# Performance work log

Measured on AMD Instinct MI355X. Metric: run time of the kernel, lower is better.

The kernel has to match this reference:

```python
import jax, jax.numpy as jnp
import numpy as np

E = 1024  # dim_model
H = 16    # num_heads
HD = E // H
B, S = 32, 2048
LN_EPS = 1e-5


def setup_inputs() -> dict:
    key = jax.random.key(0)
    ks = jax.random.split(key, 8)
    x = jax.random.normal(ks[0], (B, S, E), dtype=jnp.float32)
    key_padding_mask = jax.random.randint(ks[1], (B, S), 0, 2).astype(jnp.int32)
    # learned seed (xavier_uniform over [1,1,E])
    bound = float(np.sqrt(6.0 / (1 + E)))
    seed = jax.random.uniform(ks[2], (1, 1, E), minval=-bound, maxval=bound, dtype=jnp.float32)
    # MHA params: packed in_proj [3E, E] (q,k,v stacked) + bias, out_proj [E,E]+bias
    w_scale = 1.0 / np.sqrt(E)
    in_proj_w = jax.random.uniform(ks[3], (3 * E, E), minval=-w_scale, maxval=w_scale, dtype=jnp.float32)
    in_proj_b = jnp.zeros((3 * E,), dtype=jnp.float32)
    out_w = jax.random.uniform(ks[4], (E, E), minval=-w_scale, maxval=w_scale, dtype=jnp.float32)
    out_b = jnp.zeros((E,), dtype=jnp.float32)
    ln_g = jnp.ones((E,), dtype=jnp.float32)
    ln_b = jnp.zeros((E,), dtype=jnp.float32)
    return {"x": x, "key_padding_mask": key_padding_mask, "seed": seed,
            "in_proj_w": in_proj_w, "in_proj_b": in_proj_b,
            "out_w": out_w, "out_b": out_b, "ln_g": ln_g, "ln_b": ln_b}


def reference(x, key_padding_mask, seed, in_proj_w, in_proj_b, out_w, out_b, ln_g, ln_b):
    wq, wk, wv = in_proj_w[:E], in_proj_w[E:2 * E], in_proj_w[2 * E:]
    bq, bk, bv = in_proj_b[:E], in_proj_b[E:2 * E], in_proj_b[2 * E:]
    # q from single learned seed: [1,1,E] -> [1,H,1,HD] (broadcast over batch)
    q = (seed @ wq.T + bq).reshape(1, 1, H, HD).transpose(0, 2, 1, 3)
    k = (x @ wk.T + bk).reshape(x.shape[0], -1, H, HD).transpose(0, 2, 1, 3)  # [B,H,S,HD]
    v = (x @ wv.T + bv).reshape(x.shape[0], -1, H, HD).transpose(0, 2, 1, 3)
    scale = 1.0 / jnp.sqrt(jnp.asarray(HD, dtype=x.dtype))
    scores = jnp.einsum('bhqd,bhkd->bhqk', q * scale, k)  # broadcasts q batch dim -> [B,H,1,S]
    pad = (key_padding_mask == 0)[:, None, None, :]  # True = pad
    scores = jnp.where(pad, -jnp.inf, scores)
    attn = jax.nn.softmax(scores, axis=-1)
    ctx = jnp.einsum('bhqk,bhkd->bhqd', attn, v)  # [B,H,1,HD]
    ctx = ctx.transpose(0, 2, 1, 3).reshape(x.shape[0], E)  # squeeze single query
    out = ctx @ out_w.T + out_b
    mu = jnp.mean(out, axis=-1, keepdims=True)
    var = jnp.mean(jnp.square(out - mu), axis=-1, keepdims=True)
    return (out - mu) / jnp.sqrt(var + LN_EPS) * ln_g + ln_b
```

## Files before the change

### kernel.cpp

```cpp
#include <hip/hip_runtime.h>
#include <hip/hip_bf16.h>
#include <math.h>

#define E 1024
#define H 16
#define HD 64
#define B 32
#define S 2048
#define CH 16
#define CTOK (S / CH)
#define BHE (B * H * E)

typedef __attribute__((ext_vector_type(8))) short short8;
typedef __attribute__((ext_vector_type(4))) float f32x4;

__device__ __forceinline__ short f2bf(float f) {
    union { __hip_bfloat16 h; short s; } u;
    u.h = __float2bfloat16(f);
    return u.s;
}

__global__ __launch_bounds__(256) void qproj_kernel(const float* __restrict__ W,
                                                    const float* __restrict__ bqkv,
                                                    const float* __restrict__ seed,
                                                    float* __restrict__ q) {
    int gw = (blockIdx.x * 256 + threadIdx.x) >> 6;
    int lane = threadIdx.x & 63;
    if (gw >= E) return;
    const float4* row = (const float4*)(W + (size_t)gw * E);
    const float4* sd = (const float4*)seed;
    float acc = 0.f;
#pragma unroll
    for (int k = 0; k < 4; ++k) {
        float4 w4 = row[k * 64 + lane];
        float4 s4 = sd[k * 64 + lane];
        acc = fmaf(w4.x, s4.x, acc); acc = fmaf(w4.y, s4.y, acc);
        acc = fmaf(w4.z, s4.z, acc); acc = fmaf(w4.w, s4.w, acc);
    }
#pragma unroll
    for (int off = 32; off > 0; off >>= 1) acc += __shfl_down(acc, off, 64);
    if (lane == 0) q[gw] = acc + bqkv[gw];
}

__global__ __launch_bounds__(256) void uproj_kernel(const float* __restrict__ W,
                                                    const float* __restrict__ q,
                                                    float* __restrict__ u) {
    int h = blockIdx.y;
    int e = blockIdx.x * 256 + threadIdx.x;
    __shared__ float qs[HD];
    if (threadIdx.x < HD) qs[threadIdx.x] = q[h * HD + threadIdx.x];
    __syncthreads();
    const float* Wk = W + ((size_t)(E + h * HD)) * E + e;
    float acc = 0.f;
#pragma unroll 8
    for (int d = 0; d < HD; ++d) acc = fmaf(qs[d], Wk[(size_t)d * E], acc);
    u[h * E + e] = acc * 0.125f;
}

__global__ __launch_bounds__(512, 4) void fused_kernel(const float* __restrict__ x,
                                                       const int* __restrict__ mask,
                                                       const float* __restrict__ u,
                                                       float* __restrict__ part,
                                                       float* __restrict__ mstat,
                                                       float* __restrict__ lstat) {
    int ss = blockIdx.x, b = blockIdx.y;
    __shared__ short uB[H * E];
    __shared__ float sc[CTOK * 16];
    __shared__ int mk[CTOK];
    __shared__ float4 redm[32];
    __shared__ float mxs[16], lls[16];

    int tid = threadIdx.x;
    for (int un = tid; un < 2048; un += 512) {
        int h = un & 15, e8 = un >> 4;
        const float* up = u + (size_t)h * E + e8 * 8;
        short8 v;
#pragma unroll
        for (int j = 0; j < 8; ++j) v[j] = f2bf(up[j]);
        ((short8*)uB)[un] = v;
    }
    if (tid < CTOK) mk[tid] = mask[(size_t)b * S + ss * CTOK + tid];
    __syncthreads();

    int lane = tid & 63, wid = tid >> 6;

    {
        int tl0 = wid * 16;
        int tr = lane & 15;
        int kg = lane >> 4;
        int myTok = tl0 + tr;
        bool live = mk[myTok] != 0;
        const float* xrow = x + ((size_t)b * S + ss * CTOK + myTok) * E + kg * 8;
        const short8* uB8 = (const short8*)uB;

        f32x4 acc = {0.f, 0.f, 0.f, 0.f};
#pragma unroll 4
        for (int st = 0; st < 32; ++st) {
            float4 lo = make_float4(0.f, 0.f, 0.f, 0.f);
            float4 hi = make_float4(0.f, 0.f, 0.f, 0.f);
            if (live) {
                lo = *(const float4*)(xrow + st * 32);
                hi = *(const float4*)(xrow + st * 32 + 4);
            }
            short8 a;
            a[0] = f2bf(lo.x); a[1] = f2bf(lo.y); a[2] = f2bf(lo.z); a[3] = f2bf(lo.w);
            a[4] = f2bf(hi.x); a[5] = f2bf(hi.y); a[6] = f2bf(hi.z); a[7] = f2bf(hi.w);
            short8 bf = uB8[(st * 4 + kg) * 16 + tr];
            acc = __builtin_amdgcn_mfma_f32_16x16x32_bf16(a, bf, acc, 0, 0, 0);
        }
        int r0 = kg * 4;
#pragma unroll
        for (int r = 0; r < 4; ++r)
            sc[(tl0 + r0 + r) * 16 + tr] = acc[r];
    }
    __syncthreads();

    {
        int tok = tid >> 2, hq = tid & 3;
        float4 s4 = *(const float4*)&sc[tok * 16 + hq * 4];
        bool live = mk[tok] != 0;
        float4 sm = live ? s4 : make_float4(-1e30f, -1e30f, -1e30f, -1e30f);
#pragma unroll
        for (int off = 4; off <= 32; off <<= 1) {
            sm.x = fmaxf(sm.x, __shfl_xor(sm.x, off, 64));
            sm.y = fmaxf(sm.y, __shfl_xor(sm.y, off, 64));
            sm.z = fmaxf(sm.z, __shfl_xor(sm.z, off, 64));
            sm.w = fmaxf(sm.w, __shfl_xor(sm.w, off, 64));
        }
        if (lane < 4) redm[wid * 4 + lane] = sm;
        __syncthreads();
        if (tid < 4) {
            float4 mm = redm[tid];
#pragma unroll
            for (int w = 1; w < 8; ++w) {
                float4 v = redm[w * 4 + tid];
                mm.x = fmaxf(mm.x, v.x); mm.y = fmaxf(mm.y, v.y);
                mm.z = fmaxf(mm.z, v.z); mm.w = fmaxf(mm.w, v.w);
            }
            *(float4*)&mxs[tid * 4] = mm;
        }
        __syncthreads();
        float4 mx4 = *(const float4*)&mxs[hq * 4];
        float4 p4 = make_float4(0.f, 0.f, 0.f, 0.f);
        if (live) {
            p4.x = __expf(s4.x - mx4.x);
            p4.y = __expf(s4.y - mx4.y);
            p4.z = __expf(s4.z - mx4.z);
            p4.w = __expf(s4.w - mx4.w);
        }
        *(float4*)&sc[tok * 16 + hq * 4] = p4;
        float4 l4 = p4;
#pragma unroll
        for (int off = 4; off <= 32; off <<= 1) {
            l4.x += __shfl_xor(l4.x, off, 64);
            l4.y += __shfl_xor(l4.y, off, 64);
            l4.z += __shfl_xor(l4.z, off, 64);
            l4.w += __shfl_xor(l4.w, off, 64);
        }
        __syncthreads();
        if (lane < 4) redm[wid * 4 + lane] = l4;
        __syncthreads();
        if (tid < 4) {
            float4 sl = redm[tid];
#pragma unroll
            for (int w = 1; w < 8; ++w) {
                float4 v = redm[w * 4 + tid];
                sl.x += v.x; sl.y += v.y; sl.z += v.z; sl.w += v.w;
            }
            *(float4*)&lls[tid * 4] = sl;
        }
        __syncthreads();
        if (tid < 16) {
            mstat[((size_t)ss * B + b) * H + tid] = mxs[tid];
            lstat[((size_t)ss * B + b) * H + tid] = lls[tid];
        }
    }

    {
        float2 a2[16];
#pragma unroll
        for (int h = 0; h < 16; ++h) a2[h] = make_float2(0.f, 0.f);
        const float* xp = x + ((size_t)b * S + ss * CTOK) * E + wid * 128 + lane * 2;
        const float4* sc4 = (const float4*)sc;
        for (int tok = 0; tok < CTOK; ++tok) {
            if (!mk[tok]) continue;
            float2 xv = *(const float2*)(xp + (size_t)tok * E);
            float4 p0 = sc4[tok * 4 + 0];
            float4 p1 = sc4[tok * 4 + 1];
            float4 p2 = sc4[tok * 4 + 2];
            float4 p3 = sc4[tok * 4 + 3];
            a2[0].x = fmaf(p0.x, xv.x, a2[0].x);   a2[0].y = fmaf(p0.x, xv.y, a2[0].y);
            a2[1].x = fmaf(p0.y, xv.x, a2[1].x);   a2[1].y = fmaf(p0.y, xv.y, a2[1].y);
            a2[2].x = fmaf(p0.z, xv.x, a2[2].x);   a2[2].y = fmaf(p0.z, xv.y, a2[2].y);
            a2[3].x = fmaf(p0.w, xv.x, a2[3].x);   a2[3].y = fmaf(p0.w, xv.y, a2[3].y);
            a2[4].x = fmaf(p1.x, xv.x, a2[4].x);   a2[4].y = fmaf(p1.x, xv.y, a2[4].y);
            a2[5].x = fmaf(p1.y, xv.x, a2[5].x);   a2[5].y = fmaf(p1.y, xv.y, a2[5].y);
            a2[6].x = fmaf(p1.z, xv.x, a2[6].x);   a2[6].y = fmaf(p1.z, xv.y, a2[6].y);
            a2[7].x = fmaf(p1.w, xv.x, a2[7].x);   a2[7].y = fmaf(p1.w, xv.y, a2[7].y);
            a2[8].x = fmaf(p2.x, xv.x, a2[8].x);   a2[8].y = fmaf(p2.x, xv.y, a2[8].y);
            a2[9].x = fmaf(p2.y, xv.x, a2[9].x);   a2[9].y = fmaf(p2.y, xv.y, a2[9].y);
            a2[10].x = fmaf(p2.z, xv.x, a2[10].x); a2[10].y = fmaf(p2.z, xv.y, a2[10].y);
            a2[11].x = fmaf(p2.w, xv.x, a2[11].x); a2[11].y = fmaf(p2.w, xv.y, a2[11].y);
            a2[12].x = fmaf(p3.x, xv.x, a2[12].x); a2[12].y = fmaf(p3.x, xv.y, a2[12].y);
            a2[13].x = fmaf(p3.y, xv.x, a2[13].x); a2[13].y = fmaf(p3.y, xv.y, a2[13].y);
            a2[14].x = fmaf(p3.z, xv.x, a2[14].x); a2[14].y = fmaf(p3.z, xv.y, a2[14].y);
            a2[15].x = fmaf(p3.w, xv.x, a2[15].x); a2[15].y = fmaf(p3.w, xv.y, a2[15].y);
        }
        float* pb = part + ((size_t)ss * B + b) * (H * E) + wid * 128 + lane * 2;
#pragma unroll
        for (int h = 0; h < 16; ++h) *(float2*)(pb + (size_t)h * E) = a2[h];
    }
}

__global__ __launch_bounds__(256) void ctxc_kernel(const float* __restrict__ W,
                                                   const float* __restrict__ bqkv,
                                                   const float* __restrict__ part,
                                                   const float* __restrict__ mstat,
                                                   const float* __restrict__ lstat,
                                                   float* __restrict__ ctx) {
    int cb = blockIdx.x, b = blockIdx.y, t = threadIdx.x;
    int h0 = cb * 4;
    __shared__ float xls[4 * E];
    __shared__ float fs[4][CH];
    __shared__ float linv[4];
    if (t < 4) {
        int h = h0 + t;
        float mv[CH];
        float mg = -1e30f;
#pragma unroll
        for (int c = 0; c < CH; ++c) {
            mv[c] = mstat[((size_t)c * B + b) * H + h];
            mg = fmaxf(mg, mv[c]);
        }
        float l = 0.f;
#pragma unroll
        for (int c = 0; c < CH; ++c) {
            float fc = __expf(mv[c] - mg);
            fs[t][c] = fc;
            l = fmaf(fc, lstat[((size_t)c * B + b) * H + h], l);
        }
        linv[t] = 1.f / l;
    }
    __syncthreads();
    for (int i = t; i < 4 * E / 4; i += 256) {
        int hl = i >> 8, e4 = i & 255;
        float4 s = make_float4(0.f, 0.f, 0.f, 0.f);
#pragma unroll 4
        for (int c = 0; c < CH; ++c) {
            float fc = fs[hl][c];
            float4 v = ((const float4*)part)[(((size_t)c * B + b) * H + h0 + hl) * (E / 4) + e4];
            s.x = fmaf(fc, v.x, s.x); s.y = fmaf(fc, v.y, s.y);
            s.z = fmaf(fc, v.z, s.z); s.w = fmaf(fc, v.w, s.w);
        }
        float li = linv[hl];
        s.x *= li; s.y *= li; s.z *= li; s.w *= li;
        ((float4*)xls)[i] = s;
    }
    __syncthreads();
    int c = cb * 256 + t;
    int h = c >> 6;
    const float4* wr = (const float4*)(W + ((size_t)(2 * E + c)) * E);
    const float4* xl = (const float4*)(xls + (h - h0) * E);
    float acc = bqkv[2 * E + c];
#pragma unroll 4
    for (int e4 = 0; e4 < E / 4; ++e4) {
        float4 w = wr[e4], xv = xl[e4];
        acc = fmaf(w.x, xv.x, acc); acc = fmaf(w.y, xv.y, acc);
        acc = fmaf(w.z, xv.z, acc); acc = fmaf(w.w, xv.w, acc);
    }
    ctx[(size_t)b * E + c] = acc;
}

__global__ __launch_bounds__(256) void outproj_kernel(const float* __restrict__ Wo,
                                                      const float* __restrict__ ob,
                                                      const float* __restrict__ ctx,
                                                      float* __restrict__ outpre) {
    int obk = blockIdx.x, b = blockIdx.y, t = threadIdx.x;
    int o = obk * 256 + t;
    __shared__ float cl[E];
    const float4* cp = (const float4*)(ctx + (size_t)b * E);
    for (int i = t; i < E / 4; i += 256) ((float4*)cl)[i] = cp[i];
    __syncthreads();
    const float4* wr = (const float4*)(Wo + (size_t)o * E);
    const float4* cl4 = (const float4*)cl;
    float acc = ob[o];
#pragma unroll 4
    for (int e4 = 0; e4 < E / 4; ++e4) {
        float4 w = wr[e4], cv = cl4[e4];
        acc = fmaf(w.x, cv.x, acc); acc = fmaf(w.y, cv.y, acc);
        acc = fmaf(w.z, cv.z, acc); acc = fmaf(w.w, cv.w, acc);
    }
    outpre[(size_t)b * E + o] = acc;
}

__global__ __launch_bounds__(256) void ln_kernel(const float* __restrict__ outpre,
                                                 const float* __restrict__ g,
                                                 const float* __restrict__ bb,
                                                 float* __restrict__ out) {
    int b = blockIdx.x, t = threadIdx.x, lane = t & 63, wid = t >> 6;
    const float4* row = (const float4*)(outpre + (size_t)b * E);
    float4 v = row[t];
    float s = v.x + v.y + v.z + v.w;
    float sq = v.x * v.x + v.y * v.y + v.z * v.z + v.w * v.w;
    __shared__ float rs[4], rq[4];
#pragma unroll
    for (int off = 32; off > 0; off >>= 1) {
        s += __shfl_down(s, off, 64);
        sq += __shfl_down(sq, off, 64);
    }
    if (lane == 0) { rs[wid] = s; rq[wid] = sq; }
    __syncthreads();
    s = rs[0] + rs[1] + rs[2] + rs[3];
    sq = rq[0] + rq[1] + rq[2] + rq[3];
    float mean = s * (1.f / E);
    float var = sq * (1.f / E) - mean * mean;
    float inv = rsqrtf(var + 1e-5f);
    float4 gv = ((const float4*)g)[t];
    float4 bv = ((const float4*)bb)[t];
    float4 o;
    o.x = (v.x - mean) * inv * gv.x + bv.x;
    o.y = (v.y - mean) * inv * gv.y + bv.y;
    o.z = (v.z - mean) * inv * gv.z + bv.z;
    o.w = (v.w - mean) * inv * gv.w + bv.w;
    ((float4*)(out + (size_t)b * E))[t] = o;
}

extern "C" void kernel_launch(void* const* d_in, const int* in_sizes, int n_in,
                              void* d_out, int out_size, void* d_ws, size_t ws_size,
                              hipStream_t stream) {
    const float* x    = (const float*)d_in[0];
    const int*   mask = (const int*)d_in[1];
    const float* seed = (const float*)d_in[2];
    const float* W    = (const float*)d_in[3];
    const float* bqkv = (const float*)d_in[4];
    const float* Wo   = (const float*)d_in[5];
    const float* ob   = (const float*)d_in[6];
    const float* g    = (const float*)d_in[7];
    const float* lb   = (const float*)d_in[8];
    float* out = (float*)d_out;

    float* ws = (float*)d_ws;
    float* q      = ws;
    float* u      = q + E;
    float* part   = u + H * E;
    float* mstat  = part + (size_t)CH * BHE;
    float* lstat  = mstat + (size_t)CH * B * H;
    float* ctx    = lstat + (size_t)CH * B * H;
    float* outpre = ctx + (size_t)B * E;

    qproj_kernel<<<256, 256, 0, stream>>>(W, bqkv, seed, q);
    uproj_kernel<<<dim3(E / 256, H), 256, 0, stream>>>(W, q, u);
    fused_kernel<<<dim3(CH, B), 512, 0, stream>>>(x, mask, u, part, mstat, lstat);
    ctxc_kernel<<<dim3(E / 256, B), 256, 0, stream>>>(W, bqkv, part, mstat, lstat, ctx);
    outproj_kernel<<<dim3(E / 256, B), 256, 0, stream>>>(Wo, ob, ctx, outpre);
    ln_kernel<<<B, 256, 0, stream>>>(outpre, g, lb, out);
}
```

Before: 148.8 us.

## Stage x in bf16 shared-memory subtiles with online softmax to read x once

```diff
diff --git a/kernel.cpp b/kernel.cpp
--- a/kernel.cpp
+++ b/kernel.cpp
@@ -9,6 +9,8 @@
 #define S 2048
 #define CH 16
 #define CTOK (S / CH)
+#define SUB 32
+#define NSUB (CTOK / SUB)
 #define BHE (B * H * E)
 
 typedef __attribute__((ext_vector_type(8))) short short8;
@@ -44,7 +46,7 @@
 
 __global__ __launch_bounds__(256) void uproj_kernel(const float* __restrict__ W,
                                                     const float* __restrict__ q,
-                                                    float* __restrict__ u) {
+                                                    short* __restrict__ ubf) {
     int h = blockIdx.y;
     int e = blockIdx.x * 256 + threadIdx.x;
     __shared__ float qs[HD];
@@ -54,161 +56,158 @@
     float acc = 0.f;
 #pragma unroll 8
     for (int d = 0; d < HD; ++d) acc = fmaf(qs[d], Wk[(size_t)d * E], acc);
-    u[h * E + e] = acc * 0.125f;
+    ubf[(size_t)h * E + e] = f2bf(acc * 0.125f);
 }
 
 __global__ __launch_bounds__(512, 4) void fused_kernel(const float* __restrict__ x,
                                                        const int* __restrict__ mask,
-                                                       const float* __restrict__ u,
+                                                       const short* __restrict__ ubf,
                                                        float* __restrict__ part,
                                                        float* __restrict__ mstat,
                                                        float* __restrict__ lstat) {
     int ss = blockIdx.x, b = blockIdx.y;
-    __shared__ short uB[H * E];
-    __shared__ float sc[CTOK * 16];
-    __shared__ int mk[CTOK];
-    __shared__ float4 redm[32];
-    __shared__ float mxs[16], lls[16];
-
-    int tid = threadIdx.x;
-    for (int un = tid; un < 2048; un += 512) {
-        int h = un & 15, e8 = un >> 4;
-        const float* up = u + (size_t)h * E + e8 * 8;
-        short8 v;
-#pragma unroll
-        for (int j = 0; j < 8; ++j) v[j] = f2bf(up[j]);
-        ((short8*)uB)[un] = v;
-    }
-    if (tid < CTOK) mk[tid] = mask[(size_t)b * S + ss * CTOK + tid];
-    __syncthreads();
-
-    int lane = tid & 63, wid = tid >> 6;
-
-    {
-        int tl0 = wid * 16;
-        int tr = lane & 15;
-        int kg = lane >> 4;
-        int myTok = tl0 + tr;
-        bool live = mk[myTok] != 0;
-        const float* xrow = x + ((size_t)b * S + ss * CTOK + myTok) * E + kg * 8;
-        const short8* uB8 = (const short8*)uB;
-
-        f32x4 acc = {0.f, 0.f, 0.f, 0.f};
-#pragma unroll 4
-        for (int st = 0; st < 32; ++st) {
-            float4 lo = make_float4(0.f, 0.f, 0.f, 0.f);
-            float4 hi = make_float4(0.f, 0.f, 0.f, 0.f);
-            if (live) {
-                lo = *(const float4*)(xrow + st * 32);
-                hi = *(const float4*)(xrow + st * 32 + 4);
-            }
-            short8 a;
-            a[0] = f2bf(lo.x); a[1] = f2bf(lo.y); a[2] = f2bf(lo.z); a[3] = f2bf(lo.w);
-            a[4] = f2bf(hi.x); a[5] = f2bf(hi.y); a[6] = f2bf(hi.z); a[7] = f2bf(hi.w);
-            short8 bf = uB8[(st * 4 + kg) * 16 + tr];
-            acc = __builtin_amdgcn_mfma_f32_16x16x32_bf16(a, bf, acc, 0, 0, 0);
-        }
-        int r0 = kg * 4;
-#pragma unroll
-        for (int r = 0; r < 4; ++r)
-            sc[(tl0 + r0 + r) * 16 + tr] = acc[r];
-    }
-    __syncthreads();
-
-    {
-        int tok = tid >> 2, hq = tid & 3;
-        float4 s4 = *(const float4*)&sc[tok * 16 + hq * 4];
-        bool live = mk[tok] != 0;
-        float4 sm = live ? s4 : make_float4(-1e30f, -1e30f, -1e30f, -1e30f);
-#pragma unroll
-        for (int off = 4; off <= 32; off <<= 1) {
-            sm.x = fmaxf(sm.x, __shfl_xor(sm.x, off, 64));
-            sm.y = fmaxf(sm.y, __shfl_xor(sm.y, off, 64));
-            sm.z = fmaxf(sm.z, __shfl_xor(sm.z, off, 64));
-            sm.w = fmaxf(sm.w, __shfl_xor(sm.w, off, 64));
-        }
-        if (lane < 4) redm[wid * 4 + lane] = sm;
+    __shared__ short xB[SUB * E];
+    __shared__ float scp[8 * 64 * 4];
+    __shared__ float pcur[SUB * H];
+    __shared__ int   mk[CTOK];
+    __shared__ float mrun[H], lrun[H], rfac[H];
+    __shared__ float wred[8][16];
+
+    int tid = threadIdx.x, lane = tid & 63, wid = tid >> 6;
+
+    if (tid < H) { mrun[tid] = -1e30f; lrun[tid] = 0.f; }
+    for (int i = tid; i < CTOK; i += 512) mk[i] = mask[(size_t)b * S + ss * CTOK + i];
+
+    float2 a2[16];
+#pragma unroll
+    for (int h = 0; h < 16; ++h) a2[h] = make_float2(0.f, 0.f);
+
+    __syncthreads();
+
+    for (int sub = 0; sub < NSUB; ++sub) {
+        int t0 = sub * SUB;
+
+        {
+            int tok = tid >> 4;
+            int es  = tid & 15;
+            const float* xr = x + ((size_t)b * S + ss * CTOK + t0 + tok) * E;
+            bool live = mk[t0 + tok] != 0;
+#pragma unroll
+            for (int i = 0; i < 8; ++i) {
+                int e0 = (es + i * 16) * 8;
+                if (live) {
+                    float4 lo = *(const float4*)(xr + e0);
+                    float4 hi = *(const float4*)(xr + e0 + 4);
+                    short8 v;
+                    v[0] = f2bf(lo.x); v[1] = f2bf(lo.y); v[2] = f2bf(lo.z); v[3] = f2bf(lo.w);
+                    v[4] = f2bf(hi.x); v[5] = f2bf(hi.y); v[6] = f2bf(hi.z); v[7] = f2bf(hi.w);
+                    int byte = (tok * 2048 + e0 * 2) ^ ((tok & 7) << 4);
+                    *(short8*)((char*)xB + byte) = v;
+                }
+            }
+        }
         __syncthreads();
-        if (tid < 4) {
-            float4 mm = redm[tid];
-#pragma unroll
-            for (int w = 1; w < 8; ++w) {
-                float4 v = redm[w * 4 + tid];
-                mm.x = fmaxf(mm.x, v.x); mm.y = fmaxf(mm.y, v.y);
-                mm.z = fmaxf(mm.z, v.z); mm.w = fmaxf(mm.w, v.w);
-            }
-            *(float4*)&mxs[tid * 4] = mm;
+
+        {
+            int tw = wid & 1, kq = wid >> 1;
+            int tr = lane & 15, kg = lane >> 4;
+            int tok = tw * 16 + tr;
+            f32x4 acc = {0.f, 0.f, 0.f, 0.f};
+            const short* ub = ubf + (size_t)tr * E;
+#pragma unroll
+            for (int st = 0; st < 8; ++st) {
+                int e0 = kq * 256 + st * 32 + kg * 8;
+                int byte = (tok * 2048 + e0 * 2) ^ ((tok & 7) << 4);
+                short8 a = *(const short8*)((char*)xB + byte);
+                short8 bv = *(const short8*)(ub + e0);
+                acc = __builtin_amdgcn_mfma_f32_16x16x32_bf16(a, bv, acc, 0, 0, 0);
+            }
+            *(f32x4*)&scp[(wid * 64 + lane) * 4] = acc;
         }
         __syncthreads();
-        float4 mx4 = *(const float4*)&mxs[hq * 4];
-        float4 p4 = make_float4(0.f, 0.f, 0.f, 0.f);
-        if (live) {
-            p4.x = __expf(s4.x - mx4.x);
-            p4.y = __expf(s4.y - mx4.y);
-            p4.z = __expf(s4.z - mx4.z);
-            p4.w = __expf(s4.w - mx4.w);
-        }
-        *(float4*)&sc[tok * 16 + hq * 4] = p4;
-        float4 l4 = p4;
-#pragma unroll
-        for (int off = 4; off <= 32; off <<= 1) {
-            l4.x += __shfl_xor(l4.x, off, 64);
-            l4.y += __shfl_xor(l4.y, off, 64);
-            l4.z += __shfl_xor(l4.z, off, 64);
-            l4.w += __shfl_xor(l4.w, off, 64);
+
+        {
+            int tok = tid >> 4, h = tid & 15;
+            int tw = tok >> 4, r = tok & 3, kg2 = (tok & 15) >> 2;
+            float s = 0.f;
+#pragma unroll
+            for (int kq = 0; kq < 4; ++kq)
+                s += scp[((kq * 2 + tw) * 64 + kg2 * 16 + h) * 4 + r];
+            bool live = mk[t0 + tok] != 0;
+            float sv = live ? s : -1e30f;
+            float mx = sv;
+            mx = fmaxf(mx, __shfl_xor(mx, 16, 64));
+            mx = fmaxf(mx, __shfl_xor(mx, 32, 64));
+            if (lane < 16) wred[wid][lane] = mx;
+            __syncthreads();
+            if (tid < 16) {
+                float mt = wred[0][tid];
+#pragma unroll
+                for (int w = 1; w < 8; ++w) mt = fmaxf(mt, wred[w][tid]);
+                float mo = mrun[tid];
+                float mn = fmaxf(mo, mt);
+                rfac[tid] = __expf(mo - mn);
+                mrun[tid] = mn;
+            }
+            __syncthreads();
+            float p = live ? __expf(s - mrun[h]) : 0.f;
+            pcur[tok * 16 + h] = p;
+            float ps = p;
+            ps += __shfl_xor(ps, 16, 64);
+            ps += __shfl_xor(ps, 32, 64);
+            if (lane < 16) wred[wid][lane] = ps;
+            __syncthreads();
+            if (tid < 16) {
+                float lt = 0.f;
+#pragma unroll
+                for (int w = 0; w < 8; ++w) lt += wred[w][tid];
+                lrun[tid] = lrun[tid] * rfac[tid] + lt;
+            }
         }
         __syncthreads();
-        if (lane < 4) redm[wid * 4 + lane] = l4;
+
+        {
+#pragma unroll
+            for (int h = 0; h < 16; ++h) {
+                float r = rfac[h];
+                a2[h].x *= r; a2[h].y *= r;
+            }
+            int ebyte = tid * 4;
+            for (int tok = 0; tok < SUB; ++tok) {
+                if (!mk[t0 + tok]) continue;
+                int byte = (tok * 2048 + ebyte) ^ ((tok & 7) << 4);
+                unsigned xv2 = *(const unsigned*)((char*)xB + byte);
+                float xe0 = __uint_as_float(xv2 << 16);
+                float xe1 = __uint_as_float(xv2 & 0xffff0000u);
+                const float4* pr = (const float4*)&pcur[tok * 16];
+                float4 p0 = pr[0], p1 = pr[1], p2 = pr[2], p3 = pr[3];
+                a2[0].x = fmaf(p0.x, xe0, a2[0].x);   a2[0].y = fmaf(p0.x, xe1, a2[0].y);
+                a2[1].x = fmaf(p0.y, xe0, a2[1].x);   a2[1].y = fmaf(p0.y, xe1, a2[1].y);
+                a2[2].x = fmaf(p0.z, xe0, a2[2].x);   a2[2].y = fmaf(p0.z, xe1, a2[2].y);
+                a2[3].x = fmaf(p0.w, xe0, a2[3].x);   a2[3].y = fmaf(p0.w, xe1, a2[3].y);
+                a2[4].x = fmaf(p1.x, xe0, a2[4].x);   a2[4].y = fmaf(p1.x, xe1, a2[4].y);
+                a2[5].x = fmaf(p1.y, xe0, a2[5].x);   a2[5].y = fmaf(p1.y, xe1, a2[5].y);
+                a2[6].x = fmaf(p1.z, xe0, a2[6].x);   a2[6].y = fmaf(p1.z, xe1, a2[6].y);
+                a2[7].x = fmaf(p1.w, xe0, a2[7].x);   a2[7].y = fmaf(p1.w, xe1, a2[7].y);
+                a2[8].x = fmaf(p2.x, xe0, a2[8].x);   a2[8].y = fmaf(p2.x, xe1, a2[8].y);
+                a2[9].x = fmaf(p2.y, xe0, a2[9].x);   a2[9].y = fmaf(p2.y, xe1, a2[9].y);
+                a2[10].x = fmaf(p2.z, xe0, a2[10].x); a2[10].y = fmaf(p2.z, xe1, a2[10].y);
+                a2[11].x = fmaf(p2.w, xe0, a2[11].x); a2[11].y = fmaf(p2.w, xe1, a2[11].y);
+                a2[12].x = fmaf(p3.x, xe0, a2[12].x); a2[12].y = fmaf(p3.x, xe1, a2[12].y);
+                a2[13].x = fmaf(p3.y, xe0, a2[13].x); a2[13].y = fmaf(p3.y, xe1, a2[13].y);
+                a2[14].x = fmaf(p3.z, xe0, a2[14].x); a2[14].y = fmaf(p3.z, xe1, a2[14].y);
+                a2[15].x = fmaf(p3.w, xe0, a2[15].x); a2[15].y = fmaf(p3.w, xe1, a2[15].y);
+            }
+        }
         __syncthreads();
-        if (tid < 4) {
-            float4 sl = redm[tid];
-#pragma unroll
-            for (int w = 1; w < 8; ++w) {
-                float4 v = redm[w * 4 + tid];
-                sl.x += v.x; sl.y += v.y; sl.z += v.z; sl.w += v.w;
-            }
-            *(float4*)&lls[tid * 4] = sl;
-        }
-        __syncthreads();
-        if (tid < 16) {
-            mstat[((size_t)ss * B + b) * H + tid] = mxs[tid];
-            lstat[((size_t)ss * B + b) * H + tid] = lls[tid];
-        }
-    }
-
-    {
-        float2 a2[16];
-#pragma unroll
-        for (int h = 0; h < 16; ++h) a2[h] = make_float2(0.f, 0.f);
-        const float* xp = x + ((size_t)b * S + ss * CTOK) * E + wid * 128 + lane * 2;
-        const float4* sc4 = (const float4*)sc;
-        for (int tok = 0; tok < CTOK; ++tok) {
-            if (!mk[tok]) continue;
-            float2 xv = *(const float2*)(xp + (size_t)tok * E);
-            float4 p0 = sc4[tok * 4 + 0];
-            float4 p1 = sc4[tok * 4 + 1];
-            float4 p2 = sc4[tok * 4 + 2];
-            float4 p3 = sc4[tok * 4 + 3];
-            a2[0].x = fmaf(p0.x, xv.x, a2[0].x);   a2[0].y = fmaf(p0.x, xv.y, a2[0].y);
-            a2[1].x = fmaf(p0.y, xv.x, a2[1].x);   a2[1].y = fmaf(p0.y, xv.y, a2[1].y);
-            a2[2].x = fmaf(p0.z, xv.x, a2[2].x);   a2[2].y = fmaf(p0.z, xv.y, a2[2].y);
-            a2[3].x = fmaf(p0.w, xv.x, a2[3].x);   a2[3].y = fmaf(p0.w, xv.y, a2[3].y);
-            a2[4].x = fmaf(p1.x, xv.x, a2[4].x);   a2[4].y = fmaf(p1.x, xv.y, a2[4].y);
-            a2[5].x = fmaf(p1.y, xv.x, a2[5].x);   a2[5].y = fmaf(p1.y, xv.y, a2[5].y);
-            a2[6].x = fmaf(p1.z, xv.x, a2[6].x);   a2[6].y = fmaf(p1.z, xv.y, a2[6].y);
-            a2[7].x = fmaf(p1.w, xv.x, a2[7].x);   a2[7].y = fmaf(p1.w, xv.y, a2[7].y);
-            a2[8].x = fmaf(p2.x, xv.x, a2[8].x);   a2[8].y = fmaf(p2.x, xv.y, a2[8].y);
-            a2[9].x = fmaf(p2.y, xv.x, a2[9].x);   a2[9].y = fmaf(p2.y, xv.y, a2[9].y);
-            a2[10].x = fmaf(p2.z, xv.x, a2[10].x); a2[10].y = fmaf(p2.z, xv.y, a2[10].y);
-            a2[11].x = fmaf(p2.w, xv.x, a2[11].x); a2[11].y = fmaf(p2.w, xv.y, a2[11].y);
-            a2[12].x = fmaf(p3.x, xv.x, a2[12].x); a2[12].y = fmaf(p3.x, xv.y, a2[12].y);
-            a2[13].x = fmaf(p3.y, xv.x, a2[13].x); a2[13].y = fmaf(p3.y, xv.y, a2[13].y);
-            a2[14].x = fmaf(p3.z, xv.x, a2[14].x); a2[14].y = fmaf(p3.z, xv.y, a2[14].y);
-            a2[15].x = fmaf(p3.w, xv.x, a2[15].x); a2[15].y = fmaf(p3.w, xv.y, a2[15].y);
-        }
-        float* pb = part + ((size_t)ss * B + b) * (H * E) + wid * 128 + lane * 2;
-#pragma unroll
-        for (int h = 0; h < 16; ++h) *(float2*)(pb + (size_t)h * E) = a2[h];
+    }
+
+    float* pb = part + ((size_t)ss * B + b) * (H * E) + tid * 2;
+#pragma unroll
+    for (int h = 0; h < 16; ++h) *(float2*)(pb + (size_t)h * E) = a2[h];
+    if (tid < 16) {
+        mstat[((size_t)ss * B + b) * H + tid] = mrun[tid];
+        lstat[((size_t)ss * B + b) * H + tid] = lrun[tid];
     }
 }
 
@@ -341,16 +340,16 @@
 
     float* ws = (float*)d_ws;
     float* q      = ws;
-    float* u      = q + E;
-    float* part   = u + H * E;
+    float* part   = q + E;
     float* mstat  = part + (size_t)CH * BHE;
     float* lstat  = mstat + (size_t)CH * B * H;
-    float* ctx    = lstat + (size_t)CH * B * H;
+    short* ubf    = (short*)(lstat + (size_t)CH * B * H);
+    float* ctx    = (float*)(ubf + (size_t)H * E);
     float* outpre = ctx + (size_t)B * E;
 
     qproj_kernel<<<256, 256, 0, stream>>>(W, bqkv, seed, q);
-    uproj_kernel<<<dim3(E / 256, H), 256, 0, stream>>>(W, q, u);
-    fused_kernel<<<dim3(CH, B), 512, 0, stream>>>(x, mask, u, part, mstat, lstat);
+    uproj_kernel<<<dim3(E / 256, H), 256, 0, stream>>>(W, q, ubf);
+    fused_kernel<<<dim3(CH, B), 512, 0, stream>>>(x, mask, ubf, part, mstat, lstat);
     ctxc_kernel<<<dim3(E / 256, B), 256, 0, stream>>>(W, bqkv, part, mstat, lstat, ctx);
     outproj_kernel<<<dim3(E / 256, B), 256, 0, stream>>>(Wo, ob, ctx, outpre);
     ln_kernel<<<B, 256, 0, stream>>>(outpre, g, lb, out);
```

Result: faster. 131.3 us (-11.8%).
